# Optimization experiments

Hardware: AMD Instinct MI355X
Metric: run time of the kernel (lower is better)

Reference implementation:

```python
import jax, jax.numpy as jnp
import numpy as np

IMG_FEAT = 2048
HIDDEN = 512


def setup_inputs() -> dict:
    key = jax.random.key(0)
    ks = jax.random.split(key, 9)
    B, R = 512, 10
    img = jax.random.normal(ks[0], (B * R, IMG_FEAT), dtype=jnp.float32)
    ques = jax.random.normal(ks[1], (B * R, HIDDEN), dtype=jnp.float32)
    hist = jax.random.normal(ks[2], (B * R, R, HIDDEN), dtype=jnp.float32)
    fusion = IMG_FEAT + HIDDEN
    # kaiming-uniform-ish init scales
    W_fuse = jax.random.uniform(ks[3], (HIDDEN, fusion), dtype=jnp.float32,
                                minval=-1.0, maxval=1.0) * np.sqrt(6.0 / fusion)
    b_fuse = jnp.zeros((HIDDEN,), dtype=jnp.float32)
    w_att = jax.random.uniform(ks[4], (HIDDEN,), dtype=jnp.float32,
                               minval=-1.0, maxval=1.0) * np.sqrt(6.0 / HIDDEN)
    b_att = jnp.zeros((), dtype=jnp.float32)
    W_hist = jax.random.uniform(ks[5], (HIDDEN, HIDDEN), dtype=jnp.float32,
                                minval=-1.0, maxval=1.0) * np.sqrt(6.0 / HIDDEN)
    b_hist = jnp.zeros((HIDDEN,), dtype=jnp.float32)
    return {
        "img": img, "ques": ques, "hist": hist,
        "W_fuse": W_fuse, "b_fuse": b_fuse,
        "w_att": w_att, "b_att": b_att,
        "W_hist": W_hist, "b_hist": b_hist,
        "batch_size": B, "num_rounds": R,
    }


def reference(img, ques, hist, W_fuse, b_fuse, w_att, b_att, W_hist, b_hist,
              batch_size, num_rounds):
    # Dropout is identity (eval mode).
    BR = batch_size * num_rounds
    # fused embedding: tanh(Linear(cat(img, ques)))  -> [B*R, D]
    fused_vec = jnp.concatenate([img, ques], axis=1)
    fused = jnp.tanh(fused_vec @ W_fuse.T + b_fuse)
    D = fused.shape[-1]
    hist_r = hist.reshape(BR, num_rounds, D)  # [B*R, R, D]
    # scores: (hist * broadcast(fused)) @ w_att + b_att  -> [B*R, R]
    # equivalent to the repeat + elementwise-mul + linear-to-scalar in torch
    scores = jnp.einsum('brd,bd,d->br', hist_r, fused, w_att) + b_att
    attn = jax.nn.softmax(scores, axis=1)  # softmax over num_rounds
    hist_embed = jnp.einsum('br,brd->bd', attn, hist_r)  # weighted sum
    hist_embed = jnp.tanh(hist_embed @ W_hist.T + b_hist)
    out = fused + hist_embed
    return out.reshape(batch_size, num_rounds, D)
```

## Files before the change

### kernel.cpp

```cpp
#include <hip/hip_runtime.h>
#include <hip/hip_bf16.h>

#define HIDDEN 512
#define IMGF   2048
#define RNDS   10

typedef float  f32x4  __attribute__((ext_vector_type(4)));
typedef __bf16 bf16x8 __attribute__((ext_vector_type(8)));
typedef unsigned short u16x8 __attribute__((ext_vector_type(8)));

__device__ __forceinline__ unsigned short f2bf(float x) {
    union { float f; unsigned u; } v; v.f = x;
    unsigned r = v.u + 0x7FFFu + ((v.u >> 16) & 1u);
    return (unsigned short)(r >> 16);
}

__device__ __forceinline__ void cp16_async(const void* g, void* l) {
    __builtin_amdgcn_global_load_lds(
        (const __attribute__((address_space(1))) unsigned int*)g,
        (__attribute__((address_space(3))) unsigned int*)l,
        16, 0, 0);
}

__global__ __launch_bounds__(256)
void cvt_bf16(const float* __restrict__ p0, long n0,
              const float* __restrict__ p1, long n1,
              const float* __restrict__ p2, long n2,
              const float* __restrict__ p3, long n3,
              unsigned short* __restrict__ q0, unsigned short* __restrict__ q1,
              unsigned short* __restrict__ q2, unsigned short* __restrict__ q3)
{
    long i = ((long)blockIdx.x * 256 + threadIdx.x) * 4;
    const float* s; unsigned short* d; long j;
    if      (i < n0)            { s = p0; d = q0; j = i; }
    else if (i < n0 + n1)       { s = p1; d = q1; j = i - n0; }
    else if (i < n0 + n1 + n2)  { s = p2; d = q2; j = i - n0 - n1; }
    else                        { s = p3; d = q3; j = i - n0 - n1 - n2; }
    float4 v = *(const float4*)(s + j);
    ushort4 o;
    o.x = f2bf(v.x); o.y = f2bf(v.y); o.z = f2bf(v.z); o.w = f2bf(v.w);
    *(ushort4*)(d + j) = o;
}

template<bool RESID>
__global__ __launch_bounds__(256, 2)
void gemm_bt_tanh(const unsigned short* __restrict__ A0, int lda0,
                  const unsigned short* __restrict__ A1, int lda1, int kSplit,
                  const unsigned short* __restrict__ W,
                  const float* __restrict__ bias,
                  const float* __restrict__ resid,
                  float* __restrict__ out, int K)
{
    __shared__ unsigned short lA[2][64 * 64];
    __shared__ unsigned short lB[2][64 * 64];

    const int bm = blockIdx.x * 64;
    const int bn = blockIdx.y * 64;
    const int t    = threadIdx.x;
    const int lane = t & 63;
    const int wave = t >> 6;
    const int wm = (wave & 1) * 32;
    const int wn = (wave >> 1) * 32;
    const int lr = lane & 15;
    const int lq = lane >> 4;

    const unsigned short* Wb0 = W + (size_t)bn * K;

    auto stage64 = [&](const unsigned short* G, int lda, unsigned short* L) {
        #pragma unroll
        for (int h = 0; h < 2; ++h) {
            int ci = h * 256 + t;
            int r  = ci >> 3;
            int s  = (ci & 7) ^ (r & 7);
            cp16_async(G + (size_t)r * lda + s * 8, L + ci * 8);
        }
    };
    auto stage_tiles = [&](int kt, int buf) {
        int k0 = kt << 6;
        const unsigned short* Ab; int lda;
        if (k0 < kSplit) { Ab = A0 + (size_t)bm * lda0 + k0;            lda = lda0; }
        else             { Ab = A1 + (size_t)bm * lda1 + (k0 - kSplit); lda = lda1; }
        stage64(Ab, lda, &lA[buf][0]);
        stage64(Wb0 + k0, K, &lB[buf][0]);
    };

    f32x4 acc[2][2] = {};
    const int NT = K >> 6;

    stage_tiles(0, 0);
    for (int kt = 0; kt < NT; ++kt) {
        __syncthreads();
        if (kt + 1 < NT) stage_tiles(kt + 1, (kt + 1) & 1);
        const unsigned short* a = &lA[kt & 1][0];
        const unsigned short* b = &lB[kt & 1][0];
        #pragma unroll
        for (int kh = 0; kh < 2; ++kh) {
            bf16x8 af[2], bfr[2];
            #pragma unroll
            for (int mi = 0; mi < 2; ++mi) {
                int r = wm + mi * 16 + lr, c = kh * 4 + lq;
                af[mi] = __builtin_bit_cast(bf16x8,
                    *(const u16x8*)&a[r * 64 + ((c ^ (r & 7)) * 8)]);
            }
            #pragma unroll
            for (int ni = 0; ni < 2; ++ni) {
                int r = wn + ni * 16 + lr, c = kh * 4 + lq;
                bfr[ni] = __builtin_bit_cast(bf16x8,
                    *(const u16x8*)&b[r * 64 + ((c ^ (r & 7)) * 8)]);
            }
            #pragma unroll
            for (int mi = 0; mi < 2; ++mi)
                #pragma unroll
                for (int ni = 0; ni < 2; ++ni)
                    acc[mi][ni] = __builtin_amdgcn_mfma_f32_16x16x32_bf16(
                        af[mi], bfr[ni], acc[mi][ni], 0, 0, 0);
        }
    }

    #pragma unroll
    for (int ni = 0; ni < 2; ++ni) {
        const int col = bn + wn + ni * 16 + lr;
        const float bc = bias[col];
        #pragma unroll
        for (int mi = 0; mi < 2; ++mi) {
            const int rbase = bm + wm + mi * 16 + lq * 4;
            #pragma unroll
            for (int j = 0; j < 4; ++j) {
                const int row = rbase + j;
                float v = tanhf(acc[mi][ni][j] + bc);
                if (RESID) v += resid[(size_t)row * HIDDEN + col];
                out[(size_t)row * HIDDEN + col] = v;
            }
        }
    }
}

__global__ __launch_bounds__(256)
void attn_embed(const float* __restrict__ hist,
                const float* __restrict__ fused,
                const float* __restrict__ w_att,
                const float* __restrict__ b_att,
                unsigned short* __restrict__ hembed)
{
    const int lane = threadIdx.x & 63;
    const int wave = threadIdx.x >> 6;
    const int b = blockIdx.x * 4 + wave;
    const int d = lane * 8;

    float g[8];
    {
        const float4 f0 = *(const float4*)(fused + (size_t)b * HIDDEN + d);
        const float4 f1 = *(const float4*)(fused + (size_t)b * HIDDEN + d + 4);
        const float4 w0 = *(const float4*)(w_att + d);
        const float4 w1 = *(const float4*)(w_att + d + 4);
        g[0]=f0.x*w0.x; g[1]=f0.y*w0.y; g[2]=f0.z*w0.z; g[3]=f0.w*w0.w;
        g[4]=f1.x*w1.x; g[5]=f1.y*w1.y; g[6]=f1.z*w1.z; g[7]=f1.w*w1.w;
    }
    const float* hb = hist + (size_t)b * RNDS * HIDDEN + d;

    float h[RNDS][8], p[RNDS];
    #pragma unroll
    for (int r = 0; r < RNDS; ++r) {
        const float4 a0 = *(const float4*)(hb + r * HIDDEN);
        const float4 a1 = *(const float4*)(hb + r * HIDDEN + 4);
        h[r][0]=a0.x; h[r][1]=a0.y; h[r][2]=a0.z; h[r][3]=a0.w;
        h[r][4]=a1.x; h[r][5]=a1.y; h[r][6]=a1.z; h[r][7]=a1.w;
        float s = 0.f;
        #pragma unroll
        for (int i = 0; i < 8; ++i) s += h[r][i] * g[i];
        p[r] = s;
    }
    #pragma unroll
    for (int r = 0; r < RNDS; ++r)
        #pragma unroll
        for (int m = 1; m < 64; m <<= 1)
            p[r] += __shfl_xor(p[r], m, 64);

    const float ba = b_att[0];
    float mx = -1e30f;
    #pragma unroll
    for (int r = 0; r < RNDS; ++r) mx = fmaxf(mx, p[r] + ba);
    float sum = 0.f, a[RNDS];
    #pragma unroll
    for (int r = 0; r < RNDS; ++r) { a[r] = __expf(p[r] + ba - mx); sum += a[r]; }
    const float inv = 1.0f / sum;

    float e[8] = {};
    #pragma unroll
    for (int r = 0; r < RNDS; ++r)
        #pragma unroll
        for (int i = 0; i < 8; ++i) e[i] += a[r] * h[r][i];

    ushort4 o0, o1;
    o0.x=f2bf(e[0]*inv); o0.y=f2bf(e[1]*inv); o0.z=f2bf(e[2]*inv); o0.w=f2bf(e[3]*inv);
    o1.x=f2bf(e[4]*inv); o1.y=f2bf(e[5]*inv); o1.z=f2bf(e[6]*inv); o1.w=f2bf(e[7]*inv);
    unsigned short* q = hembed + (size_t)b * HIDDEN + d;
    *(ushort4*)q = o0;
    *(ushort4*)(q + 4) = o1;
}

extern "C" void kernel_launch(void* const* d_in, const int* in_sizes, int n_in,
                              void* d_out, int out_size, void* d_ws, size_t ws_size,
                              hipStream_t stream)
{
    const float* img    = (const float*)d_in[0];
    const float* ques   = (const float*)d_in[1];
    const float* hist   = (const float*)d_in[2];
    const float* W_fuse = (const float*)d_in[3];
    const float* b_fuse = (const float*)d_in[4];
    const float* w_att  = (const float*)d_in[5];
    const float* b_att  = (const float*)d_in[6];
    const float* W_hist = (const float*)d_in[7];
    const float* b_hist = (const float*)d_in[8];

    const long n_img  = in_sizes[0];
    const long n_ques = in_sizes[1];
    const long n_Wf   = in_sizes[3];
    const long n_Wh   = in_sizes[7];
    const int  BR     = (int)(n_ques / HIDDEN);

    unsigned short* imgb  = (unsigned short*)d_ws;
    unsigned short* quesb = imgb  + n_img;
    unsigned short* Wfb   = quesb + n_ques;
    unsigned short* Whb   = Wfb   + n_Wf;
    unsigned short* hembb = Whb   + n_Wh;
    float* fused = (float*)d_out;

    const long total4 = (n_img + n_ques + n_Wf + n_Wh) / 4;
    cvt_bf16<<<dim3((unsigned)((total4 + 255) / 256)), dim3(256), 0, stream>>>(
        img, n_img, ques, n_ques, W_fuse, n_Wf, W_hist, n_Wh,
        imgb, quesb, Wfb, Whb);

    dim3 blk(256);
    dim3 g1(BR / 64, HIDDEN / 64);

    gemm_bt_tanh<false><<<g1, blk, 0, stream>>>(
        imgb, IMGF, quesb, HIDDEN, IMGF,
        Wfb, b_fuse, nullptr, fused, IMGF + HIDDEN);

    attn_embed<<<dim3(BR / 4), blk, 0, stream>>>(hist, fused, w_att, b_att, hembb);

    gemm_bt_tanh<true><<<g1, blk, 0, stream>>>(
        hembb, HIDDEN, nullptr, 0, HIDDEN,
        Whb, b_hist, fused, (float*)d_out, HIDDEN);
}
```

Baseline: 263.2 us.

## Halve GEMM M-tile to 32 rows and store fused intermediate in bf16

The GEMM block tile shrinks from 64x64 to 32x64, so each wave computes one 16-row slice with two MFMAs per k-step. This doubles the grid (BR/32 × 8) and raises the launch bound to 4 blocks per CU, aiming to fill more CUs for this small M×N problem. The fused intermediate is now written as bf16 to workspace, which cuts bytes for the attention read and the residual read. The cost is more reloading of W tiles across blocks, and the residual carries bf16 rounding error.

```diff
diff --git a/kernel.cpp b/kernel.cpp
--- a/kernel.cpp
+++ b/kernel.cpp
@@ -13,6 +13,10 @@
     union { float f; unsigned u; } v; v.f = x;
     unsigned r = v.u + 0x7FFFu + ((v.u >> 16) & 1u);
     return (unsigned short)(r >> 16);
+}
+__device__ __forceinline__ float bf2f(unsigned short h) {
+    union { unsigned u; float f; } v; v.u = ((unsigned)h) << 16;
+    return v.f;
 }
 
 __device__ __forceinline__ void cp16_async(const void* g, void* l) {
@@ -43,48 +47,48 @@
 }
 
 template<bool RESID>
-__global__ __launch_bounds__(256, 2)
+__global__ __launch_bounds__(256, 4)
 void gemm_bt_tanh(const unsigned short* __restrict__ A0, int lda0,
                   const unsigned short* __restrict__ A1, int lda1, int kSplit,
                   const unsigned short* __restrict__ W,
                   const float* __restrict__ bias,
-                  const float* __restrict__ resid,
-                  float* __restrict__ out, int K)
-{
-    __shared__ unsigned short lA[2][64 * 64];
+                  const unsigned short* __restrict__ residb,
+                  float* __restrict__ outf, unsigned short* __restrict__ outb,
+                  int K)
+{
+    __shared__ unsigned short lA[2][32 * 64];
     __shared__ unsigned short lB[2][64 * 64];
 
-    const int bm = blockIdx.x * 64;
+    const int bm = blockIdx.x * 32;
     const int bn = blockIdx.y * 64;
     const int t    = threadIdx.x;
     const int lane = t & 63;
     const int wave = t >> 6;
-    const int wm = (wave & 1) * 32;
-    const int wn = (wave >> 1) * 32;
+    const int wm = (wave >> 1) * 16;
+    const int wn = (wave & 1) * 32;
     const int lr = lane & 15;
     const int lq = lane >> 4;
 
     const unsigned short* Wb0 = W + (size_t)bn * K;
 
-    auto stage64 = [&](const unsigned short* G, int lda, unsigned short* L) {
-        #pragma unroll
-        for (int h = 0; h < 2; ++h) {
-            int ci = h * 256 + t;
-            int r  = ci >> 3;
-            int s  = (ci & 7) ^ (r & 7);
-            cp16_async(G + (size_t)r * lda + s * 8, L + ci * 8);
-        }
-    };
     auto stage_tiles = [&](int kt, int buf) {
         int k0 = kt << 6;
         const unsigned short* Ab; int lda;
         if (k0 < kSplit) { Ab = A0 + (size_t)bm * lda0 + k0;            lda = lda0; }
         else             { Ab = A1 + (size_t)bm * lda1 + (k0 - kSplit); lda = lda1; }
-        stage64(Ab, lda, &lA[buf][0]);
-        stage64(Wb0 + k0, K, &lB[buf][0]);
+        {
+            int r = t >> 3, s = (t & 7) ^ (r & 7);
+            cp16_async(Ab + (size_t)r * lda + s * 8, &lA[buf][t * 8]);
+        }
+        #pragma unroll
+        for (int h = 0; h < 2; ++h) {
+            int ci = h * 256 + t;
+            int r = ci >> 3, s = (ci & 7) ^ (r & 7);
+            cp16_async(Wb0 + k0 + (size_t)r * K + s * 8, &lB[buf][ci * 8]);
+        }
     };
 
-    f32x4 acc[2][2] = {};
+    f32x4 acc[2] = {};
     const int NT = K >> 6;
 
     stage_tiles(0, 0);
@@ -95,25 +99,18 @@
         const unsigned short* b = &lB[kt & 1][0];
         #pragma unroll
         for (int kh = 0; kh < 2; ++kh) {
-            bf16x8 af[2], bfr[2];
-            #pragma unroll
-            for (int mi = 0; mi < 2; ++mi) {
-                int r = wm + mi * 16 + lr, c = kh * 4 + lq;
-                af[mi] = __builtin_bit_cast(bf16x8,
-                    *(const u16x8*)&a[r * 64 + ((c ^ (r & 7)) * 8)]);
-            }
+            const int c = kh * 4 + lq;
+            const int ra = wm + lr;
+            bf16x8 af = __builtin_bit_cast(bf16x8,
+                *(const u16x8*)&a[ra * 64 + ((c ^ (ra & 7)) * 8)]);
             #pragma unroll
             for (int ni = 0; ni < 2; ++ni) {
-                int r = wn + ni * 16 + lr, c = kh * 4 + lq;
-                bfr[ni] = __builtin_bit_cast(bf16x8,
-                    *(const u16x8*)&b[r * 64 + ((c ^ (r & 7)) * 8)]);
+                const int rb = wn + ni * 16 + lr;
+                bf16x8 bf = __builtin_bit_cast(bf16x8,
+                    *(const u16x8*)&b[rb * 64 + ((c ^ (rb & 7)) * 8)]);
+                acc[ni] = __builtin_amdgcn_mfma_f32_16x16x32_bf16(
+                    af, bf, acc[ni], 0, 0, 0);
             }
-            #pragma unroll
-            for (int mi = 0; mi < 2; ++mi)
-                #pragma unroll
-                for (int ni = 0; ni < 2; ++ni)
-                    acc[mi][ni] = __builtin_amdgcn_mfma_f32_16x16x32_bf16(
-                        af[mi], bfr[ni], acc[mi][ni], 0, 0, 0);
         }
     }
 
@@ -121,23 +118,20 @@
     for (int ni = 0; ni < 2; ++ni) {
         const int col = bn + wn + ni * 16 + lr;
         const float bc = bias[col];
-        #pragma unroll
-        for (int mi = 0; mi < 2; ++mi) {
-            const int rbase = bm + wm + mi * 16 + lq * 4;
-            #pragma unroll
-            for (int j = 0; j < 4; ++j) {
-                const int row = rbase + j;
-                float v = tanhf(acc[mi][ni][j] + bc);
-                if (RESID) v += resid[(size_t)row * HIDDEN + col];
-                out[(size_t)row * HIDDEN + col] = v;
-            }
+        const int rbase = bm + wm + lq * 4;
+        #pragma unroll
+        for (int j = 0; j < 4; ++j) {
+            const size_t idx = (size_t)(rbase + j) * HIDDEN + col;
+            float v = tanhf(acc[ni][j] + bc);
+            if (RESID) outf[idx] = v + bf2f(residb[idx]);
+            else       outb[idx] = f2bf(v);
         }
     }
 }
 
 __global__ __launch_bounds__(256)
 void attn_embed(const float* __restrict__ hist,
-                const float* __restrict__ fused,
+                const unsigned short* __restrict__ fusedb,
                 const float* __restrict__ w_att,
                 const float* __restrict__ b_att,
                 unsigned short* __restrict__ hembed)
@@ -149,12 +143,11 @@
 
     float g[8];
     {
-        const float4 f0 = *(const float4*)(fused + (size_t)b * HIDDEN + d);
-        const float4 f1 = *(const float4*)(fused + (size_t)b * HIDDEN + d + 4);
+        u16x8 f = *(const u16x8*)(fusedb + (size_t)b * HIDDEN + d);
         const float4 w0 = *(const float4*)(w_att + d);
         const float4 w1 = *(const float4*)(w_att + d + 4);
-        g[0]=f0.x*w0.x; g[1]=f0.y*w0.y; g[2]=f0.z*w0.z; g[3]=f0.w*w0.w;
-        g[4]=f1.x*w1.x; g[5]=f1.y*w1.y; g[6]=f1.z*w1.z; g[7]=f1.w*w1.w;
+        g[0]=bf2f(f[0])*w0.x; g[1]=bf2f(f[1])*w0.y; g[2]=bf2f(f[2])*w0.z; g[3]=bf2f(f[3])*w0.w;
+        g[4]=bf2f(f[4])*w1.x; g[5]=bf2f(f[5])*w1.y; g[6]=bf2f(f[6])*w1.z; g[7]=bf2f(f[7])*w1.w;
     }
     const float* hb = hist + (size_t)b * RNDS * HIDDEN + d;
 
@@ -219,12 +212,12 @@
     const long n_Wh   = in_sizes[7];
     const int  BR     = (int)(n_ques / HIDDEN);
 
-    unsigned short* imgb  = (unsigned short*)d_ws;
-    unsigned short* quesb = imgb  + n_img;
-    unsigned short* Wfb   = quesb + n_ques;
-    unsigned short* Whb   = Wfb   + n_Wf;
-    unsigned short* hembb = Whb   + n_Wh;
-    float* fused = (float*)d_out;
+    unsigned short* imgb   = (unsigned short*)d_ws;
+    unsigned short* quesb  = imgb   + n_img;
+    unsigned short* Wfb    = quesb  + n_ques;
+    unsigned short* Whb    = Wfb    + n_Wf;
+    unsigned short* fusedb = Whb    + n_Wh;
+    unsigned short* hembb  = fusedb + (size_t)BR * HIDDEN;
 
     const long total4 = (n_img + n_ques + n_Wf + n_Wh) / 4;
     cvt_bf16<<<dim3((unsigned)((total4 + 255) / 256)), dim3(256), 0, stream>>>(
@@ -232,15 +225,15 @@
         imgb, quesb, Wfb, Whb);
 
     dim3 blk(256);
-    dim3 g1(BR / 64, HIDDEN / 64);
+    dim3 g1(BR / 32, HIDDEN / 64);
 
     gemm_bt_tanh<false><<<g1, blk, 0, stream>>>(
         imgb, IMGF, quesb, HIDDEN, IMGF,
-        Wfb, b_fuse, nullptr, fused, IMGF + HIDDEN);
-
-    attn_embed<<<dim3(BR / 4), blk, 0, stream>>>(hist, fused, w_att, b_att, hembb);
+        Wfb, b_fuse, nullptr, nullptr, fusedb, IMGF + HIDDEN);
+
+    attn_embed<<<dim3(BR / 4), blk, 0, stream>>>(hist, fusedb, w_att, b_att, hembb);
 
     gemm_bt_tanh<true><<<g1, blk, 0, stream>>>(
         hembb, HIDDEN, nullptr, 0, HIDDEN,
-        Whb, b_hist, fused, (float*)d_out, HIDDEN);
-}
+        Whb, b_hist, fusedb, (float*)d_out, nullptr, HIDDEN);
+}
```

Measured after the change: 257.0 us. 1.02x faster.
